# Performance work log

Measured on AMD Instinct MI355X. Metric: run time of the kernel, lower is better.

The kernel has to match this reference:

```python
import jax, jax.numpy as jnp
import numpy as np
from jax import lax

B, H, W, CIN = 16, 96, 320, 32
N_ACTIVE = 200000
COUT = 256
FC_IN = (H // 8) * (W // 8) * 128  # 12*40*128 = 61440


def _conv(x, w, b):
    # stride-2, pad-1, 3x3 conv in NCHW / OIHW layout
    y = lax.conv_general_dilated(x, w, (2, 2), [(1, 1), (1, 1)],
                                 dimension_numbers=('NCHW', 'OIHW', 'NCHW'))
    return y + b[None, :, None, None]


def _maxpool3(x):
    # 3x3 maxpool, stride 1, pad 1 (NCHW)
    return lax.reduce_window(x, -jnp.inf, lax.max,
                             (1, 1, 3, 3), (1, 1, 1, 1),
                             [(0, 0), (0, 0), (1, 1), (1, 1)])


def setup_inputs() -> dict:
    key = jax.random.key(0)
    ks = jax.random.split(key, 12)
    input_feat = jax.random.normal(ks[0], (B, H, W, CIN), dtype=jnp.float32)
    cb = jax.random.randint(ks[1], (N_ACTIVE, 1), 0, B)
    cy = jax.random.randint(ks[2], (N_ACTIVE, 1), 0, H)
    cx = jax.random.randint(ks[3], (N_ACTIVE, 1), 0, W)
    spconv_coords = jnp.concatenate([cb, cy, cx], axis=1).astype(jnp.int32)
    w1 = jax.random.normal(ks[4], (32, CIN, 3, 3), dtype=jnp.float32) * (1.0 / np.sqrt(CIN * 9))
    b1 = jax.random.normal(ks[5], (32,), dtype=jnp.float32) * 0.01
    w2 = jax.random.normal(ks[6], (64, 32, 3, 3), dtype=jnp.float32) * (1.0 / np.sqrt(32 * 9))
    b2 = jax.random.normal(ks[7], (64,), dtype=jnp.float32) * 0.01
    w3 = jax.random.normal(ks[8], (128, 64, 3, 3), dtype=jnp.float32) * (1.0 / np.sqrt(64 * 9))
    b3 = jax.random.normal(ks[9], (128,), dtype=jnp.float32) * 0.01
    fc_w = jax.random.normal(ks[10], (COUT, FC_IN), dtype=jnp.float32) * (1.0 / np.sqrt(FC_IN))
    fc_b = jax.random.normal(ks[11], (COUT,), dtype=jnp.float32) * 0.01
    return {"input_feat": input_feat, "spconv_coords": spconv_coords,
            "w1": w1, "b1": b1, "w2": w2, "b2": b2, "w3": w3, "b3": b3,
            "fc_w": fc_w, "fc_b": fc_b}


def reference(input_feat, spconv_coords, w1, b1, w2, b2, w3, b3, fc_w, fc_b):
    bi = spconv_coords[:, 0]
    yi = spconv_coords[:, 1]
    xi = spconv_coords[:, 2]
    # gather active-site features, then scatter into a dense NHWC grid
    feats = input_feat[bi, yi, xi]                       # [N, CIN]
    dense = jnp.zeros_like(input_feat).at[bi, yi, xi].set(feats)
    x = dense.transpose(0, 3, 1, 2)                      # [B, CIN, H, W]
    x = jax.nn.relu(_maxpool3(_conv(x, w1, b1)))         # [B, 32, H/2, W/2]
    x = jax.nn.relu(_maxpool3(_conv(x, w2, b2)))         # [B, 64, H/4, W/4]
    x = jax.nn.relu(_maxpool3(_conv(x, w3, b3)))         # [B, 128, H/8, W/8]
    x = x.reshape(x.shape[0], -1)                        # [B, FC_IN]
    return jax.nn.relu(x @ fc_w.T + fc_b)                # [B, COUT]
```

## Files before the change

kernel.cpp:

```cpp
#include <hip/hip_runtime.h>

#define NB 16
#define NH 96
#define NW 320
#define NCIN 32

typedef __attribute__((ext_vector_type(8))) short short8;
typedef __attribute__((ext_vector_type(4))) float f32x4;

__device__ inline unsigned short f2bf(float f) {
    union { float f; unsigned int u; } v; v.f = f;
    unsigned int r = v.u + 0x7FFF + ((v.u >> 16) & 1);
    return (unsigned short)(r >> 16);
}

__global__ __launch_bounds__(256) void setup_all(const float* __restrict__ w1,
                                                 const float* __restrict__ w2,
                                                 const float* __restrict__ w3,
                                                 unsigned short* __restrict__ f1,
                                                 unsigned short* __restrict__ f2,
                                                 unsigned short* __restrict__ f3,
                                                 const int* __restrict__ coords,
                                                 const float* __restrict__ input,
                                                 unsigned short* __restrict__ inBf,
                                                 int n) {
    if (blockIdx.x < 396) {
        int i = blockIdx.x * 256 + threadIdx.x;
        if (i < 9216) {
            int j = i & 7, lane = (i >> 3) & 63, nt = (i >> 9) & 1, tap = i >> 10;
            int ic = ((lane >> 4) * 8) + j, oc = nt * 16 + (lane & 15);
            f1[i] = f2bf(w1[(oc * 32 + ic) * 9 + tap]);
        } else if (i < 27648) {
            int v = i - 9216;
            int j = v & 7, lane = (v >> 3) & 63, nt = (v >> 9) & 3, tap = v >> 11;
            int ic = ((lane >> 4) * 8) + j, oc = nt * 16 + (lane & 15);
            f2[v] = f2bf(w2[(oc * 32 + ic) * 9 + tap]);
        } else if (i < 101376) {
            int v = i - 27648;
            int j = v & 7, lane = (v >> 3) & 63, nt = (v >> 9) & 7, kk = v >> 12;
            int tap = kk >> 1, ks = kk & 1;
            int ic = ks * 32 + ((lane >> 4) * 8) + j, oc = nt * 16 + (lane & 15);
            f3[v] = f2bf(w3[(oc * 64 + ic) * 9 + tap]);
        }
    } else {
        int i = (blockIdx.x - 396) * 256 + threadIdx.x;
        if (i >= n * 4) return;
        int ci = i >> 2, q = i & 3;
        int b = coords[ci * 3 + 0], y = coords[ci * 3 + 1], x = coords[ci * 3 + 2];
        long base = ((long)((b * NH + y) * NW + x)) * NCIN + q * 8;
        const float4* src = (const float4*)(input + base);
        float4 v0 = src[0], v1 = src[1];
        union { short8 s8; unsigned short us[8]; } o;
        o.us[0] = f2bf(v0.x); o.us[1] = f2bf(v0.y); o.us[2] = f2bf(v0.z); o.us[3] = f2bf(v0.w);
        o.us[4] = f2bf(v1.x); o.us[5] = f2bf(v1.y); o.us[6] = f2bf(v1.z); o.us[7] = f2bf(v1.w);
        *(short8*)(inBf + base) = o.s8;
    }
}

template<int IC, int OC, int NL, int IH, int IW, int OH, int OW>
__global__ __launch_bounds__(256) void conv_mfma(
    const unsigned short* __restrict__ inPtr,
    const unsigned short* __restrict__ wfrag,
    const float* __restrict__ bias,
    float* __restrict__ out)
{
    constexpr int KS = IC / 32;
    constexpr int NT = OC / 16;
    constexpr int NG = NT / NL;
    constexpr int NSTRIPS = NB * OH * OW / 16;

    const int wid  = (blockIdx.x * 256 + threadIdx.x) >> 6;
    const int lane = threadIdx.x & 63;
    const int ntb  = (wid % NG) * NL;
    const int s    = wid / NG;
    if (s >= NSTRIPS) return;
    const int quad = lane >> 4;
    const int lm   = lane & 15;

    const int p0 = s * 16;
    const int posA = p0 + lm;
    const int b  = posA / (OH * OW);
    const int rr = posA % (OH * OW);
    const int oy = rr / OW, ox = rr % OW;
    const int iy0 = oy * 2 - 1, ix0 = ox * 2 - 1;

    int cell[9];
    bool okb[9];
    #pragma unroll
    for (int t9 = 0; t9 < 9; t9++) {
        const int iy = iy0 + t9 / 3;
        const int ix = ix0 + t9 % 3;
        const bool ok = (iy >= 0) && (iy < IH) && (ix >= 0) && (ix < IW);
        cell[t9] = ok ? ((b * IH + iy) * IW + ix) : 0;
        okb[t9] = ok;
    }

    short8 zero8;
    #pragma unroll
    for (int j = 0; j < 8; j++) zero8[j] = 0;

    f32x4 acc[NL][2];
    #pragma unroll
    for (int nl = 0; nl < NL; nl++)
        #pragma unroll
        for (int pp = 0; pp < 2; pp++)
            acc[nl][pp] = (f32x4){0.f, 0.f, 0.f, 0.f};

    #pragma unroll 1
    for (int ks = 0; ks < KS; ks++) {
        short8 av[9];
        #pragma unroll
        for (int t9 = 0; t9 < 9; t9++) {
            short8 v = *(const short8*)(inPtr + (long)cell[t9] * IC + ks * 32 + quad * 8);
            av[t9] = okb[t9] ? v : zero8;
        }
        #pragma unroll
        for (int nl = 0; nl < NL; nl++) {
            #pragma unroll
            for (int t9 = 0; t9 < 9; t9++) {
                short8 bf = *(const short8*)(wfrag + (((t9 * KS + ks) * NT + ntb + nl) * 64 + lane) * 8);
                if (t9 & 1) acc[nl][1] = __builtin_amdgcn_mfma_f32_16x16x32_bf16(av[t9], bf, acc[nl][1], 0, 0, 0);
                else        acc[nl][0] = __builtin_amdgcn_mfma_f32_16x16x32_bf16(av[t9], bf, acc[nl][0], 0, 0, 0);
            }
        }
    }

    const long rowBase = (long)p0 + quad * 4;
    #pragma unroll
    for (int nl = 0; nl < NL; nl++) {
        const int oc = (ntb + nl) * 16 + lm;
        const float bv = bias[oc];
        #pragma unroll
        for (int reg = 0; reg < 4; reg++)
            out[(rowBase + reg) * OC + oc] = acc[nl][0][reg] + acc[nl][1][reg] + bv;
    }
}

template<int C, int HH, int WW, bool BF16OUT>
__global__ __launch_bounds__(256) void maxpool3_relu(const float* __restrict__ in, void* __restrict__ outv) {
    constexpr int C4 = C / 4;
    int i = blockIdx.x * blockDim.x + threadIdx.x;
    if (i >= NB * HH * WW * C4) return;
    int c = i % C4;
    int x = (i / C4) % WW;
    int y = (i / (C4 * WW)) % HH;
    int b = i / (C4 * WW * HH);
    float4 m = make_float4(-3.0e38f, -3.0e38f, -3.0e38f, -3.0e38f);
    #pragma unroll
    for (int dy = -1; dy <= 1; dy++) {
        int yy = y + dy;
        if (yy < 0 || yy >= HH) continue;
        #pragma unroll
        for (int dx = -1; dx <= 1; dx++) {
            int xx = x + dx;
            if (xx < 0 || xx >= WW) continue;
            float4 v = ((const float4*)in)[((b * HH + yy) * WW + xx) * C4 + c];
            m.x = fmaxf(m.x, v.x);
            m.y = fmaxf(m.y, v.y);
            m.z = fmaxf(m.z, v.z);
            m.w = fmaxf(m.w, v.w);
        }
    }
    m.x = fmaxf(m.x, 0.f);
    m.y = fmaxf(m.y, 0.f);
    m.z = fmaxf(m.z, 0.f);
    m.w = fmaxf(m.w, 0.f);
    if (BF16OUT) {
        ushort4 o;
        o.x = f2bf(m.x); o.y = f2bf(m.y); o.z = f2bf(m.z); o.w = f2bf(m.w);
        ((ushort4*)outv)[i] = o;
    } else {
        ((float4*)outv)[i] = m;
    }
}

__global__ __launch_bounds__(256) void transpose_fc(const float* __restrict__ in, float* __restrict__ xT) {
    __shared__ float tile_s[32 * 16 * 17];
    const int pt = blockIdx.x % 30;
    const int ct = blockIdx.x / 30;
    const int pos0 = pt * 16, c0 = ct * 32;
    const int t = threadIdx.x;
    {
        const int b = t / 16, pl = t % 16;
        const float4* src = (const float4*)(in + ((long)(b * 480 + pos0 + pl)) * 128 + c0);
        #pragma unroll
        for (int q = 0; q < 8; q++) {
            float4 v = src[q];
            tile_s[((4 * q + 0) * 16 + pl) * 17 + b] = v.x;
            tile_s[((4 * q + 1) * 16 + pl) * 17 + b] = v.y;
            tile_s[((4 * q + 2) * 16 + pl) * 17 + b] = v.z;
            tile_s[((4 * q + 3) * 16 + pl) * 17 + b] = v.w;
        }
    }
    __syncthreads();
    {
        const int w = t / 64, l = t % 64;
        const int pl2 = l / 4, b4 = l % 4;
        #pragma unroll
        for (int i = 0; i < 8; i++) {
            int cl = w + 4 * i;
            const float* ls = &tile_s[(cl * 16 + pl2) * 17 + 4 * b4];
            float4 v = make_float4(ls[0], ls[1], ls[2], ls[3]);
            *(float4*)(xT + ((long)(c0 + cl) * 480 + pos0 + pl2) * 16 + 4 * b4) = v;
        }
    }
}

__global__ __launch_bounds__(256) void fc_stage1(const float* __restrict__ xT,
                                                 const float* __restrict__ fw,
                                                 float* __restrict__ partial)
{
    __shared__ float red[32 * 257];
    const int tile  = blockIdx.x / 15;
    const int chunk = blockIdx.x % 15;
    const int t = threadIdx.x;
    const int K = 61440, KC = 4096;

    float acc[4][16];
    #pragma unroll
    for (int o = 0; o < 4; o++)
        #pragma unroll
        for (int bb = 0; bb < 16; bb++) acc[o][bb] = 0.f;

    const int k0 = chunk * KC;
    #pragma unroll 2
    for (int k = k0 + t; k < k0 + KC; k += 256) {
        const float4* xp = (const float4*)(xT + (long)k * 16);
        float4 x0 = xp[0], x1 = xp[1], x2 = xp[2], x3 = xp[3];
        #pragma unroll
        for (int o = 0; o < 4; o++) {
            float w = fw[(long)(tile * 4 + o) * K + k];
            acc[o][0]  = fmaf(w, x0.x, acc[o][0]);
            acc[o][1]  = fmaf(w, x0.y, acc[o][1]);
            acc[o][2]  = fmaf(w, x0.z, acc[o][2]);
            acc[o][3]  = fmaf(w, x0.w, acc[o][3]);
            acc[o][4]  = fmaf(w, x1.x, acc[o][4]);
            acc[o][5]  = fmaf(w, x1.y, acc[o][5]);
            acc[o][6]  = fmaf(w, x1.z, acc[o][6]);
            acc[o][7]  = fmaf(w, x1.w, acc[o][7]);
            acc[o][8]  = fmaf(w, x2.x, acc[o][8]);
            acc[o][9]  = fmaf(w, x2.y, acc[o][9]);
            acc[o][10] = fmaf(w, x2.z, acc[o][10]);
            acc[o][11] = fmaf(w, x2.w, acc[o][11]);
            acc[o][12] = fmaf(w, x3.x, acc[o][12]);
            acc[o][13] = fmaf(w, x3.y, acc[o][13]);
            acc[o][14] = fmaf(w, x3.z, acc[o][14]);
            acc[o][15] = fmaf(w, x3.w, acc[o][15]);
        }
    }

    #pragma unroll
    for (int oo = 0; oo < 2; oo++)
        #pragma unroll
        for (int bb = 0; bb < 16; bb++)
            red[(oo * 16 + bb) * 257 + t] = acc[oo][bb];
    __syncthreads();
    if (t < 32) {
        float s = 0.f;
        for (int i = 0; i < 256; i++) s += red[t * 257 + i];
        partial[((long)chunk * 256 + tile * 4 + (t / 16)) * 16 + (t % 16)] = s;
    }
    __syncthreads();
    #pragma unroll
    for (int oo = 0; oo < 2; oo++)
        #pragma unroll
        for (int bb = 0; bb < 16; bb++)
            red[(oo * 16 + bb) * 257 + t] = acc[2 + oo][bb];
    __syncthreads();
    if (t < 32) {
        float s = 0.f;
        for (int i = 0; i < 256; i++) s += red[t * 257 + i];
        partial[((long)chunk * 256 + tile * 4 + 2 + (t / 16)) * 16 + (t % 16)] = s;
    }
}

__global__ __launch_bounds__(256) void fc_reduce(const float* __restrict__ partial,
                                                 const float* __restrict__ fcb,
                                                 float* __restrict__ out)
{
    int i = blockIdx.x * blockDim.x + threadIdx.x;
    if (i >= 4096) return;
    int oc = i / 16, b = i % 16;
    float s = fcb[oc];
    #pragma unroll
    for (int c = 0; c < 15; c++) s += partial[(c * 256 + oc) * 16 + b];
    out[b * 256 + oc] = fmaxf(s, 0.f);
}

extern "C" void kernel_launch(void* const* d_in, const int* in_sizes, int n_in,
                              void* d_out, int out_size, void* d_ws, size_t ws_size,
                              hipStream_t stream) {
    const float* input  = (const float*)d_in[0];
    const int*   coords = (const int*)d_in[1];
    const float* w1 = (const float*)d_in[2];
    const float* b1 = (const float*)d_in[3];
    const float* w2 = (const float*)d_in[4];
    const float* b2 = (const float*)d_in[5];
    const float* w3 = (const float*)d_in[6];
    const float* b3 = (const float*)d_in[7];
    const float* fcw = (const float*)d_in[8];
    const float* fcb = (const float*)d_in[9];
    float* outp = (float*)d_out;

    const int n_active = in_sizes[1] / 3;

    char* ws = (char*)d_ws;
    unsigned short* wf1 = (unsigned short*)ws;
    unsigned short* wf2 = wf1 + 9216;
    unsigned short* wf3 = wf2 + 18432;
    unsigned short* inBf = (unsigned short*)(ws + 204800);
    char* regA = ws + 204800 + 31457280;
    char* regB = regA + 15728640;
    float* partial = (float*)(regB + 7864320);

    float*          conv1o  = (float*)regA;
    unsigned short* pool1bf = (unsigned short*)regB;
    float*          conv2o  = (float*)regA;
    unsigned short* pool2bf = (unsigned short*)regB;
    float*          conv3o  = (float*)regA;
    float*          pool3f  = (float*)regB;
    float*          xT      = (float*)regA;

    hipMemsetAsync(inBf, 0, 31457280, stream);
    const int scatterBlocks = (n_active * 4 + 255) / 256;
    setup_all<<<396 + scatterBlocks, 256, 0, stream>>>(w1, w2, w3, wf1, wf2, wf3,
                                                       coords, input, inBf, n_active);

    conv_mfma<32, 32, 2, 96, 320, 48, 160>
        <<<1920, 256, 0, stream>>>(inBf, wf1, b1, conv1o);
    maxpool3_relu<32, 48, 160, true><<<3840, 256, 0, stream>>>(conv1o, pool1bf);

    conv_mfma<32, 64, 2, 48, 160, 24, 80>
        <<<960, 256, 0, stream>>>(pool1bf, wf2, b2, conv2o);
    maxpool3_relu<64, 24, 80, true><<<1920, 256, 0, stream>>>(conv2o, pool2bf);

    conv_mfma<64, 128, 2, 24, 80, 12, 40>
        <<<480, 256, 0, stream>>>(pool2bf, wf3, b3, conv3o);
    maxpool3_relu<128, 12, 40, false><<<960, 256, 0, stream>>>(conv3o, pool3f);

    transpose_fc<<<120, 256, 0, stream>>>(pool3f, xT);
    fc_stage1<<<960, 256, 0, stream>>>(xT, fcw, partial);
    fc_reduce<<<16, 256, 0, stream>>>(partial, fcb, outp);
}
```

Measured before the change: 247.8 us.

## Restructure FC split-K so each thread owns one output channel

The fully connected layer is rewritten so that each block handles a 120-element slice of K and each thread computes one output channel. A thread holds its weight slice in registers, and the activations are read through block-uniform broadcast loads. This removes the old shared-memory cross-thread reduction and its barriers. In exchange, the partial-sum buffer grows to 512 chunks, and fc_reduce becomes a per-channel block reduction with more global traffic. Weight reads are now strided across lanes rather than coalesced, and the larger partial buffer must fit in the workspace.

```diff
diff --git a/kernel.cpp b/kernel.cpp
--- a/kernel.cpp
+++ b/kernel.cpp
@@ -4,6 +4,10 @@
 #define NH 96
 #define NW 320
 #define NCIN 32
+
+#define FC_K 61440
+#define FC_KC 120
+#define FC_NCHUNK 512
 
 typedef __attribute__((ext_vector_type(8))) short short8;
 typedef __attribute__((ext_vector_type(4))) float f32x4;
@@ -206,85 +210,63 @@
     }
 }
 
-__global__ __launch_bounds__(256) void fc_stage1(const float* __restrict__ xT,
-                                                 const float* __restrict__ fw,
-                                                 float* __restrict__ partial)
+__global__ __launch_bounds__(256) void fc_main(const float* __restrict__ xT,
+                                               const float* __restrict__ fw,
+                                               float* __restrict__ partial)
 {
-    __shared__ float red[32 * 257];
-    const int tile  = blockIdx.x / 15;
-    const int chunk = blockIdx.x % 15;
-    const int t = threadIdx.x;
-    const int K = 61440, KC = 4096;
-
-    float acc[4][16];
-    #pragma unroll
-    for (int o = 0; o < 4; o++)
-        #pragma unroll
-        for (int bb = 0; bb < 16; bb++) acc[o][bb] = 0.f;
-
-    const int k0 = chunk * KC;
-    #pragma unroll 2
-    for (int k = k0 + t; k < k0 + KC; k += 256) {
-        const float4* xp = (const float4*)(xT + (long)k * 16);
-        float4 x0 = xp[0], x1 = xp[1], x2 = xp[2], x3 = xp[3];
-        #pragma unroll
-        for (int o = 0; o < 4; o++) {
-            float w = fw[(long)(tile * 4 + o) * K + k];
-            acc[o][0]  = fmaf(w, x0.x, acc[o][0]);
-            acc[o][1]  = fmaf(w, x0.y, acc[o][1]);
-            acc[o][2]  = fmaf(w, x0.z, acc[o][2]);
-            acc[o][3]  = fmaf(w, x0.w, acc[o][3]);
-            acc[o][4]  = fmaf(w, x1.x, acc[o][4]);
-            acc[o][5]  = fmaf(w, x1.y, acc[o][5]);
-            acc[o][6]  = fmaf(w, x1.z, acc[o][6]);
-            acc[o][7]  = fmaf(w, x1.w, acc[o][7]);
-            acc[o][8]  = fmaf(w, x2.x, acc[o][8]);
-            acc[o][9]  = fmaf(w, x2.y, acc[o][9]);
-            acc[o][10] = fmaf(w, x2.z, acc[o][10]);
-            acc[o][11] = fmaf(w, x2.w, acc[o][11]);
-            acc[o][12] = fmaf(w, x3.x, acc[o][12]);
-            acc[o][13] = fmaf(w, x3.y, acc[o][13]);
-            acc[o][14] = fmaf(w, x3.z, acc[o][14]);
-            acc[o][15] = fmaf(w, x3.w, acc[o][15]);
-        }
-    }
-
-    #pragma unroll
-    for (int oo = 0; oo < 2; oo++)
-        #pragma unroll
-        for (int bb = 0; bb < 16; bb++)
-            red[(oo * 16 + bb) * 257 + t] = acc[oo][bb];
-    __syncthreads();
-    if (t < 32) {
-        float s = 0.f;
-        for (int i = 0; i < 256; i++) s += red[t * 257 + i];
-        partial[((long)chunk * 256 + tile * 4 + (t / 16)) * 16 + (t % 16)] = s;
-    }
-    __syncthreads();
-    #pragma unroll
-    for (int oo = 0; oo < 2; oo++)
-        #pragma unroll
-        for (int bb = 0; bb < 16; bb++)
-            red[(oo * 16 + bb) * 257 + t] = acc[2 + oo][bb];
-    __syncthreads();
-    if (t < 32) {
-        float s = 0.f;
-        for (int i = 0; i < 256; i++) s += red[t * 257 + i];
-        partial[((long)chunk * 256 + tile * 4 + 2 + (t / 16)) * 16 + (t % 16)] = s;
-    }
+    const int c  = blockIdx.x;
+    const int oc = threadIdx.x;
+    const int k0 = c * FC_KC;
+
+    const float4* wp = (const float4*)(fw + (long)oc * FC_K + k0);
+    float4 w[30];
+    #pragma unroll
+    for (int i = 0; i < 30; i++) w[i] = wp[i];
+
+    float acc[16];
+    #pragma unroll
+    for (int b = 0; b < 16; b++) acc[b] = 0.f;
+
+    const float* xb = xT + (long)k0 * 16;
+    #pragma unroll
+    for (int g = 0; g < 30; g++) {
+        #pragma unroll
+        for (int j = 0; j < 4; j++) {
+            const float wv = (j == 0) ? w[g].x : (j == 1) ? w[g].y : (j == 2) ? w[g].z : w[g].w;
+            const float* xp = xb + (g * 4 + j) * 16;
+            #pragma unroll
+            for (int b = 0; b < 16; b++)
+                acc[b] = fmaf(wv, xp[b], acc[b]);
+        }
+    }
+
+    float4* pp = (float4*)(partial + ((long)c * 256 + oc) * 16);
+    pp[0] = make_float4(acc[0],  acc[1],  acc[2],  acc[3]);
+    pp[1] = make_float4(acc[4],  acc[5],  acc[6],  acc[7]);
+    pp[2] = make_float4(acc[8],  acc[9],  acc[10], acc[11]);
+    pp[3] = make_float4(acc[12], acc[13], acc[14], acc[15]);
 }
 
 __global__ __launch_bounds__(256) void fc_reduce(const float* __restrict__ partial,
                                                  const float* __restrict__ fcb,
                                                  float* __restrict__ out)
 {
-    int i = blockIdx.x * blockDim.x + threadIdx.x;
-    if (i >= 4096) return;
-    int oc = i / 16, b = i % 16;
-    float s = fcb[oc];
-    #pragma unroll
-    for (int c = 0; c < 15; c++) s += partial[(c * 256 + oc) * 16 + b];
-    out[b * 256 + oc] = fmaxf(s, 0.f);
+    __shared__ float red[16][17];
+    const int oc = blockIdx.x;
+    const int ol = threadIdx.x & 15;
+    const int st = threadIdx.x >> 4;
+    float s = 0.f;
+    #pragma unroll
+    for (int j = 0; j < 32; j++)
+        s += partial[(long)(st + 16 * j) * 4096 + oc * 16 + ol];
+    red[st][ol] = s;
+    __syncthreads();
+    if (threadIdx.x < 16) {
+        float tot = fcb[oc];
+        #pragma unroll
+        for (int k = 0; k < 16; k++) tot += red[k][threadIdx.x];
+        out[threadIdx.x * 256 + oc] = fmaxf(tot, 0.f);
+    }
 }
 
 extern "C" void kernel_launch(void* const* d_in, const int* in_sizes, int n_in,
@@ -339,6 +321,6 @@
     maxpool3_relu<128, 12, 40, false><<<960, 256, 0, stream>>>(conv3o, pool3f);
 
     transpose_fc<<<120, 256, 0, stream>>>(pool3f, xT);
-    fc_stage1<<<960, 256, 0, stream>>>(xT, fcw, partial);
-    fc_reduce<<<16, 256, 0, stream>>>(partial, fcb, outp);
-}
+    fc_main<<<FC_NCHUNK, 256, 0, stream>>>(xT, fcw, partial);
+    fc_reduce<<<256, 256, 0, stream>>>(partial, fcb, outp);
+}
```

Measured after the change: 243.8 us. Within noise of the previous version (-1.6%).
